# Kernel optimization log

Hardware: AMD Instinct MI355X
Metric: run time of the kernel (lower is better)

The kernel has to match this reference:

```python
import jax, jax.numpy as jnp
import numpy as np

B, N, C, K = 2, 8192, 128, 16
EPS = 1e-5


def setup_inputs() -> dict:
    key = jax.random.key(0)
    ks = jax.random.split(key, 24)
    s = 1.0 / np.sqrt(C)
    nrm = lambda k, shape, sc: jax.random.normal(k, shape, dtype=jnp.float32) * sc
    return {
        "xyz": jax.random.normal(ks[0], (B, N, 3), dtype=jnp.float32),
        "feat": jax.random.normal(ks[1], (B, N, C), dtype=jnp.float32),
        "Wq": nrm(ks[2], (C, C), s),
        "Wk": nrm(ks[3], (C, C), s),
        "Wv": nrm(ks[4], (C, C), s),
        "pW1": nrm(ks[5], (C, 3), 0.5),
        "pb1": nrm(ks[6], (C,), 0.1),
        "pg": jnp.ones((C,), jnp.float32),
        "pbeta": jnp.zeros((C,), jnp.float32),
        "pmean": nrm(ks[7], (C,), 0.1),
        "pvar": jax.random.uniform(ks[8], (C,), jnp.float32, 0.5, 1.5),
        "pW2": nrm(ks[9], (C, C), s),
        "pb2": nrm(ks[10], (C,), 0.1),
        "aW1": nrm(ks[11], (C, C), s),
        "ab1": nrm(ks[12], (C,), 0.1),
        "ag": jnp.ones((C,), jnp.float32),
        "abeta": jnp.zeros((C,), jnp.float32),
        "amean": nrm(ks[13], (C,), 0.1),
        "avar": jax.random.uniform(ks[14], (C,), jnp.float32, 0.5, 1.5),
        "aW2": nrm(ks[15], (C, C), s),
        "ab2": nrm(ks[16], (C,), 0.1),
        "Wout": nrm(ks[17], (C, C), s),
    }


def _bn(x, g, b, mean, var):
    # eval-mode BatchNorm1d with running stats
    return (x - mean) * jax.lax.rsqrt(var + EPS) * g + b


def _lin(x, W):
    # torch nn.Linear convention: W is [out, in]
    return jnp.einsum('...i,oi->...o', x, W)


def reference(xyz, feat, Wq, Wk, Wv, pW1, pb1, pg, pbeta, pmean, pvar, pW2, pb2,
              aW1, ab1, ag, abeta, amean, avar, aW2, ab2, Wout):
    # KNN via squared distances (||a||^2 + ||b||^2 - 2 a.b), [B,N,N]
    sq = jnp.sum(xyz * xyz, axis=-1)
    dist = sq[:, :, None] + sq[:, None, :] - 2.0 * jnp.einsum('bnd,bmd->bnm', xyz, xyz)
    _, idx = jax.lax.top_k(-dist, K)  # [B,N,K] nearest neighbors

    gather = jax.vmap(lambda pts, i: pts[i])  # [B,N,C],[B,N,K] -> [B,N,K,C]
    nb_xyz = gather(xyz, idx)    # [B,N,K,3]
    nb_feat = gather(feat, idx)  # [B,N,K,C]

    q = _lin(feat, Wq)[:, :, None, :]  # [B,N,1,C]
    k = _lin(nb_feat, Wk)              # [B,N,K,C]
    v = _lin(nb_feat, Wv)              # [B,N,K,C]

    rel = nb_xyz - xyz[:, :, None, :]  # [B,N,K,3]
    pos = _lin(jax.nn.relu(_bn(_lin(rel, pW1) + pb1, pg, pbeta, pmean, pvar)), pW2) + pb2

    attn = q - k + pos
    attn = _lin(jax.nn.relu(_bn(_lin(attn, aW1) + ab1, ag, abeta, amean, avar)), aW2) + ab2
    attn = jax.nn.softmax(attn, axis=2)  # per-channel softmax over K neighbors

    out = jnp.sum(attn * (v + pos), axis=2)  # [B,N,C]
    return _lin(out, Wout)
```

## Files before the change

kernel.cpp:

```cpp
#include <hip/hip_runtime.h>
#include <cstdint>
#include <cstddef>

#define BB 2
#define NN 8192
#define CC 128
#define KK 16
#define EPSV 1e-5f
#define GRP 16
#define GPTS 512
#define GCAP 32

typedef unsigned long long u64;
typedef unsigned int u32;
typedef unsigned short ushort_t;
typedef short short8v __attribute__((ext_vector_type(8)));
typedef float f32x4 __attribute__((ext_vector_type(4)));

__device__ __forceinline__ float med3f(float x, float y, float z) {
  float r;
  asm("v_med3_f32 %0, %1, %2, %3" : "=v"(r) : "v"(x), "v"(y), "v"(z));
  return r;
}

__global__ __launch_bounds__(256) void k_prep(const float* __restrict__ xyz,
                                              float4* __restrict__ xyzw) {
  int t = blockIdx.x * 256 + threadIdx.x;
  if (t >= BB * NN) return;
  float x = xyz[t * 3 + 0], y = xyz[t * 3 + 1], z = xyz[t * 3 + 2];
  float sq = __fadd_rn(__fadd_rn(__fmul_rn(x, x), __fmul_rn(y, y)), __fmul_rn(z, z));
  xyzw[t] = make_float4(x, y, z, sq);
}

__device__ __forceinline__ float distf(const float4& q, const float4& c) {
  float dot = __fadd_rn(__fadd_rn(__fmul_rn(q.x, c.x), __fmul_rn(q.y, c.y)),
                        __fmul_rn(q.z, c.z));
  float d = __fsub_rn(__fadd_rn(q.w, c.w), __fmul_rn(2.0f, dot));
  return fmaxf(d, 0.0f);
}

__device__ __forceinline__ float distq(const float4& p, const float4& c) {
  return fmaf(p.z, c.z, fmaf(p.y, c.y, fmaf(p.x, c.x, p.w + c.w)));
}

__global__ __launch_bounds__(256) void k_thr(const float4* __restrict__ xyzw,
                                             float* __restrict__ thr) {
  __shared__ float part[16][16][16];
  const int tid = threadIdx.x;
  const int qloc = tid & 15;
  const int s = tid >> 4;
  const int n = blockIdx.x * 16 + qloc;
  const int b = n >> 13;
  const float4 q = xyzw[n];
  const float4 p = make_float4(-2.f * q.x, -2.f * q.y, -2.f * q.z, q.w);
  const float4* base = xyzw + b * NN;
  float a[KK];
#pragma unroll
  for (int i = 0; i < KK; ++i) a[i] = 3.4e38f;
  const int j0 = s * 64;
#pragma unroll 4
  for (int i = 0; i < 64; ++i) {
    const float4 c = base[(j0 + i) * 8];
    const float d = distq(p, c);
#pragma unroll
    for (int k = KK - 1; k >= 1; --k) a[k] = med3f(d, a[k - 1], a[k]);
    a[0] = fminf(d, a[0]);
  }
#pragma unroll
  for (int i = 0; i < KK; ++i) part[qloc][s][i] = a[i];
  __syncthreads();
  if (s < 4) {
#pragma unroll
    for (int ss = 1; ss < 4; ++ss)
#pragma unroll
      for (int i = 0; i < KK; ++i) {
        const float d = part[qloc][s + ss * 4][i];
#pragma unroll
        for (int k = KK - 1; k >= 1; --k) a[k] = med3f(d, a[k - 1], a[k]);
        a[0] = fminf(d, a[0]);
      }
#pragma unroll
    for (int i = 0; i < KK; ++i) part[qloc][s][i] = a[i];
  }
  __syncthreads();
  if (s == 0) {
#pragma unroll
    for (int ss = 1; ss < 4; ++ss)
#pragma unroll
      for (int i = 0; i < KK; ++i) {
        const float d = part[qloc][ss][i];
#pragma unroll
        for (int k = KK - 1; k >= 1; --k) a[k] = med3f(d, a[k - 1], a[k]);
        a[0] = fminf(d, a[0]);
      }
    const float t = a[KK - 1];
    thr[n] = t + (5e-4f + 4e-5f * fabsf(t));
  }
}

__global__ __launch_bounds__(256) void k_collect(const float4* __restrict__ xyzw,
                                                 const float* __restrict__ thr,
                                                 u32* __restrict__ cnt8,
                                                 u32* __restrict__ list) {
  __shared__ float4 pts[GPTS];
  const int tid = threadIdx.x;
  const int n = blockIdx.x * 256 + tid;
  const int b = n >> 13;
  const int g = blockIdx.y;
  const int m0 = g * GPTS;
#pragma unroll
  for (int i = 0; i < GPTS / 256; ++i)
    pts[i * 256 + tid] = xyzw[b * NN + m0 + i * 256 + tid];
  const float4 q = xyzw[n];
  const float4 p = make_float4(-2.f * q.x, -2.f * q.y, -2.f * q.z, q.w);
  const float tn = thr[n];
  __syncthreads();
  u32* seg = list + ((size_t)n * GRP + g) * GCAP;
  int cnt = 0;
#pragma unroll 4
  for (int mi = 0; mi < GPTS; ++mi) {
    const float d = distq(p, pts[mi]);
    if (d <= tn) {
      if (cnt < GCAP) seg[cnt] = (u32)(m0 + mi);
      ++cnt;
    }
  }
  cnt8[n * GRP + g] = (u32)cnt;
}

__global__ __launch_bounds__(256) void k_fin(const float4* __restrict__ xyzw,
                                             const u32* __restrict__ cnt8,
                                             const u32* __restrict__ list,
                                             int* __restrict__ idx) {
  __shared__ double part[16][16][16];
  const int tid = threadIdx.x;
  const int qloc = tid & 15;
  const int s = tid >> 4;
  const int n = blockIdx.x * 16 + qloc;
  const int b = n >> 13;
  const float4 q = xyzw[n];
  const int cn = (int)cnt8[n * GRP + s];
  const int cl = (cn < GCAP) ? cn : GCAP;
  const u32* L = list + ((size_t)n * GRP + s) * GCAP;
  double keys[KK];
#pragma unroll
  for (int i = 0; i < KK; ++i) keys[i] = __longlong_as_double(0x7FEFFFFFFFFFFFFFLL);
  for (int j = 0; j < cl; ++j) {
    const u32 m = L[j];
    const float d = distf(q, xyzw[b * NN + m]);
    u64 kb_ = ((u64)__float_as_uint(d) << 32) | m;
    double kd = __longlong_as_double((long long)kb_);
    if (kd < keys[KK - 1]) {
#pragma unroll
      for (int i = 0; i < KK; ++i) {
        double lo = fmin(keys[i], kd);
        kd = fmax(keys[i], kd);
        keys[i] = lo;
      }
    }
  }
#pragma unroll
  for (int i = 0; i < KK; ++i) part[qloc][s][i] = keys[i];
  __syncthreads();
  if (s < 4) {
#pragma unroll
    for (int ss = 1; ss < 4; ++ss)
#pragma unroll
      for (int i = 0; i < KK; ++i) {
        double kd = part[qloc][s + ss * 4][i];
        if (kd < keys[KK - 1]) {
#pragma unroll
          for (int k = 0; k < KK; ++k) {
            double lo = fmin(keys[k], kd);
            kd = fmax(keys[k], kd);
            keys[k] = lo;
          }
        }
      }
#pragma unroll
    for (int i = 0; i < KK; ++i) part[qloc][s][i] = keys[i];
  }
  __syncthreads();
  if (s == 0) {
#pragma unroll
    for (int ss = 1; ss < 4; ++ss)
#pragma unroll
      for (int i = 0; i < KK; ++i) {
        double kd = part[qloc][ss][i];
        if (kd < keys[KK - 1]) {
#pragma unroll
          for (int k = 0; k < KK; ++k) {
            double lo = fmin(keys[k], kd);
            kd = fmax(keys[k], kd);
            keys[k] = lo;
          }
        }
      }
    bool ovf = false;
#pragma unroll
    for (int gg = 0; gg < GRP; ++gg) ovf |= (cnt8[n * GRP + gg] > GCAP);
    if (ovf) {
#pragma unroll
      for (int i = 0; i < KK; ++i) keys[i] = __longlong_as_double(0x7FEFFFFFFFFFFFFFLL);
      for (int mi = 0; mi < NN; ++mi) {
        const float d = distf(q, xyzw[b * NN + mi]);
        u64 kb_ = ((u64)__float_as_uint(d) << 32) | (u32)mi;
        double kd = __longlong_as_double((long long)kb_);
        if (kd < keys[KK - 1]) {
#pragma unroll
          for (int k = 0; k < KK; ++k) {
            double lo = fmin(keys[k], kd);
            kd = fmax(keys[k], kd);
            keys[k] = lo;
          }
        }
      }
    }
#pragma unroll
    for (int j = 0; j < KK; ++j)
      idx[n * KK + j] = (int)((u64)__double_as_longlong(keys[j]) & 0xffffffffu);
  }
}

__global__ __launch_bounds__(128) void k_fold(const float* __restrict__ aW1,
                                              const float* __restrict__ Wq,
                                              const float* __restrict__ Wk,
                                              const float* __restrict__ pW2,
                                              const float* __restrict__ pb2,
                                              float* __restrict__ WqA,
                                              float* __restrict__ WkA,
                                              float* __restrict__ WpA,
                                              float* __restrict__ tvec) {
  const int bx = blockIdx.x;
  const int j = threadIdx.x;
  if (bx == 48) {
    float s = 0.f;
    for (int i = 0; i < 128; ++i) s = fmaf(aW1[j * 128 + i], pb2[i], s);
    tvec[j] = s;
    return;
  }
  const int mat = bx >> 4;
  const int c0 = (bx & 15) * 8;
  const float* S = (mat == 0) ? Wq : (mat == 1) ? Wk : pW2;
  float* D = (mat == 0) ? WqA : (mat == 1) ? WkA : WpA;
  float acc[8];
#pragma unroll
  for (int r = 0; r < 8; ++r) acc[r] = 0.f;
  for (int i = 0; i < 128; ++i) {
    float sv = S[i * 128 + j];
#pragma unroll
    for (int r = 0; r < 8; ++r) acc[r] = fmaf(aW1[(c0 + r) * 128 + i], sv, acc[r]);
  }
#pragma unroll
  for (int r = 0; r < 8; ++r) D[(c0 + r) * 128 + j] = acc[r];
}

__device__ __forceinline__ void splitf(float a, ushort_t& h, ushort_t& l) {
  u32 ab = __float_as_uint(a);
  h = (ushort_t)(ab >> 16);
  float hif = __uint_as_float(ab & 0xffff0000u);
  l = (ushort_t)(__float_as_uint(a - hif) >> 16);
}

__global__ __launch_bounds__(256) void k_packw(
    const float* __restrict__ S0, const float* __restrict__ S1,
    const float* __restrict__ S2, const float* __restrict__ S3,
    const float* __restrict__ S4, const float* __restrict__ S5,
    const float* __restrict__ S6, ushort_t* __restrict__ Phall,
    ushort_t* __restrict__ Plall) {
  const int bx = blockIdx.x;
  const int mat = bx >> 3;
  const int T = bx & 7;
  const float* S;
  switch (mat) {
    case 0: S = S0; break;
    case 1: S = S1; break;
    case 2: S = S2; break;
    case 3: S = S3; break;
    case 4: S = S4; break;
    case 5: S = S5; break;
    default: S = S6; break;
  }
  const int tid = threadIdx.x;
  const int s = tid >> 4;
  const int lr = tid & 15;
  const int c = T * 16 + lr;
  short8v vh, vl;
#pragma unroll
  for (int e = 0; e < 8; ++e) {
    ushort_t hh, ll;
    splitf(S[c * 128 + s * 8 + e], hh, ll);
    vh[e] = (short)hh;
    vl[e] = (short)ll;
  }
  const int po = mat * 16384 + T * 2048 + s * 128 + lr * 8;
  *(short8v*)&Phall[po] = vh;
  *(short8v*)&Plall[po] = vl;
}

template <int ITERS>
__device__ __forceinline__ void stage_rows(const float4* __restrict__ G4,
                                           ushort_t* Bh, ushort_t* Bl, int tid) {
#pragma unroll
  for (int i = 0; i < ITERS; ++i) {
    int f = i * 256 + tid;
    int r = f >> 5, k4 = f & 31;
    float4 v = G4[f];
    ushort_t h0, l0, h1, l1, h2, l2, h3, l3;
    splitf(v.x, h0, l0);
    splitf(v.y, h1, l1);
    splitf(v.z, h2, l2);
    splitf(v.w, h3, l3);
    int slot = k4 >> 1;
    int sub = (k4 & 1) * 4;
    int base = r * 128 + ((slot ^ (r & 15)) * 8) + sub;
    *(uint2*)&Bh[base] = make_uint2((u32)h0 | ((u32)h1 << 16), (u32)h2 | ((u32)h3 << 16));
    *(uint2*)&Bl[base] = make_uint2((u32)l0 | ((u32)l1 << 16), (u32)l2 | ((u32)l3 << 16));
  }
}

__device__ __forceinline__ void gemm64g(const ushort_t* ABh, const ushort_t* ABl,
                                        const ushort_t* __restrict__ Ph,
                                        const ushort_t* __restrict__ Pl,
                                        f32x4 acc[2][4], int tid) {
  const int l = tid & 63, wid = tid >> 6;
  const int wrow = wid >> 1, wcol = wid & 1;
  const int lq = l >> 4, lr = l & 15;
#pragma unroll
  for (int ks = 0; ks < 4; ++ks) {
    const int sw8 = (((ks * 4 + lq) ^ lr) * 8);
    short8v ah[2], al[2], wh[4], wl[4];
#pragma unroll
    for (int ct = 0; ct < 4; ++ct) {
      int off = (wcol * 4 + ct) * 2048 + (ks * 4 + lq) * 128 + lr * 8;
      wh[ct] = *(const short8v*)&Ph[off];
      wl[ct] = *(const short8v*)&Pl[off];
    }
#pragma unroll
    for (int rt = 0; rt < 2; ++rt) {
      int row = wrow * 32 + rt * 16 + lr;
      ah[rt] = *(const short8v*)&ABh[row * 128 + sw8];
      al[rt] = *(const short8v*)&ABl[row * 128 + sw8];
    }
    __builtin_amdgcn_s_setprio(1);
#pragma unroll
    for (int rt = 0; rt < 2; ++rt)
#pragma unroll
      for (int ct = 0; ct < 4; ++ct) {
        acc[rt][ct] = __builtin_amdgcn_mfma_f32_16x16x32_bf16(ah[rt], wh[ct], acc[rt][ct], 0, 0, 0);
        acc[rt][ct] = __builtin_amdgcn_mfma_f32_16x16x32_bf16(ah[rt], wl[ct], acc[rt][ct], 0, 0, 0);
        acc[rt][ct] = __builtin_amdgcn_mfma_f32_16x16x32_bf16(al[rt], wh[ct], acc[rt][ct], 0, 0, 0);
      }
    __builtin_amdgcn_s_setprio(0);
  }
}

template <int NW>
__global__ __launch_bounds__(256) void k_mms(const float* __restrict__ A,
                                             const ushort_t* __restrict__ Phall,
                                             const ushort_t* __restrict__ Plall,
                                             int m0, float* __restrict__ C0,
                                             float* __restrict__ C1,
                                             float* __restrict__ C2) {
  __shared__ ushort_t ABh[16 * 128], ABl[16 * 128];
  const int tid = threadIdx.x;
  const int Rbase = blockIdx.x * 16;
  stage_rows<2>((const float4*)(A + (size_t)Rbase * 128), ABh, ABl, tid);
  __syncthreads();
  const int l = tid & 63, wid = tid >> 6;
  const int lq = l >> 4, lr = l & 15;
  float* Cs[3] = {C0, C1, C2};
#pragma unroll
  for (int w = 0; w < NW; ++w) {
    const ushort_t* Ph = Phall + (size_t)(m0 + w) * 16384;
    const ushort_t* Pl = Plall + (size_t)(m0 + w) * 16384;
    f32x4 acc[2];
#pragma unroll
    for (int ct = 0; ct < 2; ++ct) acc[ct] = (f32x4)0.f;
#pragma unroll
    for (int ks = 0; ks < 4; ++ks) {
      const int sw8 = (((ks * 4 + lq) ^ lr) * 8);
      short8v ah, al, wh[2], wl[2];
#pragma unroll
      for (int ct = 0; ct < 2; ++ct) {
        int off = (wid * 2 + ct) * 2048 + (ks * 4 + lq) * 128 + lr * 8;
        wh[ct] = *(const short8v*)&Ph[off];
        wl[ct] = *(const short8v*)&Pl[off];
      }
      ah = *(const short8v*)&ABh[lr * 128 + sw8];
      al = *(const short8v*)&ABl[lr * 128 + sw8];
#pragma unroll
      for (int ct = 0; ct < 2; ++ct) {
        acc[ct] = __builtin_amdgcn_mfma_f32_16x16x32_bf16(ah, wh[ct], acc[ct], 0, 0, 0);
        acc[ct] = __builtin_amdgcn_mfma_f32_16x16x32_bf16(ah, wl[ct], acc[ct], 0, 0, 0);
        acc[ct] = __builtin_amdgcn_mfma_f32_16x16x32_bf16(al, wh[ct], acc[ct], 0, 0, 0);
      }
    }
#pragma unroll
    for (int ct = 0; ct < 2; ++ct) {
      int c = (wid * 2 + ct) * 16 + lr;
#pragma unroll
      for (int reg = 0; reg < 4; ++reg) {
        int R = Rbase + lq * 4 + reg;
        Cs[w][(size_t)R * 128 + c] = acc[ct][reg];
      }
    }
  }
}

__global__ __launch_bounds__(256, 3) void k_fused(
    const float4* __restrict__ xyzw, const int* __restrict__ idx,
    const float* __restrict__ qbA, const float* __restrict__ kbA,
    const float* __restrict__ vb, const float* __restrict__ pW1,
    const float* __restrict__ pb1, const float* __restrict__ pg,
    const float* __restrict__ pbeta, const float* __restrict__ pm,
    const float* __restrict__ pv, const float* __restrict__ pb2,
    const float* __restrict__ ab1, const float* __restrict__ ag,
    const float* __restrict__ abeta, const float* __restrict__ am,
    const float* __restrict__ av, const float* __restrict__ ab2,
    const float* __restrict__ tvec, const ushort_t* __restrict__ Phall,
    const ushort_t* __restrict__ Plall, float* __restrict__ outb) {
  __shared__ ushort_t ABh[64 * 128], ABl[64 * 128];
  __shared__ float4 fW1[128];
  __shared__ float sA[128], tA[128], pB2[128], aB2[128];
  __shared__ int idxs[64];
  const int tid = threadIdx.x;
  const int Qbase = blockIdx.x * 4;
  const int b = Qbase >> 13;

  if (tid < 64) idxs[tid] = idx[Qbase * KK + tid];
  if (tid < 128) {
    int c = tid;
    float s1 = pg[c] / sqrtf(pv[c] + EPSV);
    fW1[c] = make_float4(pW1[c * 3] * s1, pW1[c * 3 + 1] * s1, pW1[c * 3 + 2] * s1,
                         (pb1[c] - pm[c]) * s1 + pbeta[c]);
    float s2 = ag[c] / sqrtf(av[c] + EPSV);
    sA[c] = s2;
    tA[c] = fmaf(s2, ab1[c] + tvec[c] - am[c], abeta[c]);
    pB2[c] = pb2[c];
    aB2[c] = ab2[c];
  }
  __syncthreads();

  {
    int r = tid >> 2, qq = tid & 3;
    int Q = Qbase + (r >> 4);
    int m = idxs[r];
    float4 pq = xyzw[Q];
    float4 pn = xyzw[b * NN + m];
    float rx = pn.x - pq.x, ry = pn.y - pq.y, rz = pn.z - pq.z;
#pragma unroll
    for (int g = 0; g < 4; ++g) {
      short8v vh, vl;
      int c0 = qq * 32 + g * 8;
#pragma unroll
      for (int e = 0; e < 8; ++e) {
        float4 w = fW1[c0 + e];
        float h = fmaxf(fmaf(rz, w.z, fmaf(ry, w.y, fmaf(rx, w.x, w.w))), 0.f);
        ushort_t hh, ll;
        splitf(h, hh, ll);
        vh[e] = (short)hh;
        vl[e] = (short)ll;
      }
      int sw = (c0 >> 3) ^ (r & 15);
      *(short8v*)&ABh[r * 128 + sw * 8] = vh;
      *(short8v*)&ABl[r * 128 + sw * 8] = vl;
    }
  }
  __syncthreads();

  const int l = tid & 63, wid = tid >> 6;
  const int wrow = wid >> 1, wcol = wid & 1;
  const int lq = l >> 4, lr = l & 15;

  f32x4 pos_[2][4], pa_[2][4];
#pragma unroll
  for (int rt = 0; rt < 2; ++rt)
#pragma unroll
    for (int ct = 0; ct < 4; ++ct) {
      pos_[rt][ct] = (f32x4)0.f;
      pa_[rt][ct] = (f32x4)0.f;
    }
  gemm64g(ABh, ABl, Phall, Plall, pos_, tid);
  gemm64g(ABh, ABl, Phall + 16384, Plall + 16384, pa_, tid);
  __syncthreads();

#pragma unroll
  for (int rt = 0; rt < 2; ++rt) {
    int qi_loc = wrow * 2 + rt;
    int Q = Qbase + qi_loc;
    int mr[4];
#pragma unroll
    for (int reg = 0; reg < 4; ++reg) mr[reg] = b * NN + idxs[qi_loc * 16 + lq * 4 + reg];
#pragma unroll
    for (int ct = 0; ct < 4; ++ct) {
      int c = wcol * 64 + ct * 16 + lr;
      float qv = qbA[(size_t)Q * 128 + c];
      float sc = sA[c], tc = tA[c];
#pragma unroll
      for (int reg = 0; reg < 4; ++reg) {
        float u = qv - kbA[(size_t)mr[reg] * 128 + c] + pa_[rt][ct][reg];
        float z = fmaxf(fmaf(u, sc, tc), 0.f);
        ushort_t hh, ll;
        splitf(z, hh, ll);
        int R15 = lq * 4 + reg;
        int row = wrow * 32 + rt * 16 + R15;
        int base = row * 128 + (((c >> 3) ^ R15) * 8) + (c & 7);
        ABh[base] = hh;
        ABl[base] = ll;
      }
    }
  }
  __syncthreads();

  f32x4 acc[2][4];
#pragma unroll
  for (int rt = 0; rt < 2; ++rt)
#pragma unroll
    for (int ct = 0; ct < 4; ++ct) acc[rt][ct] = (f32x4)0.f;
  gemm64g(ABh, ABl, Phall + 32768, Plall + 32768, acc, tid);

#pragma unroll
  for (int rt = 0; rt < 2; ++rt) {
    int qi_loc = wrow * 2 + rt;
    int Q = Qbase + qi_loc;
    int mr[4];
#pragma unroll
    for (int reg = 0; reg < 4; ++reg) mr[reg] = b * NN + idxs[qi_loc * 16 + lq * 4 + reg];
#pragma unroll
    for (int ct = 0; ct < 4; ++ct) {
      int c = wcol * 64 + ct * 16 + lr;
      float ab2v = aB2[c];
      float lg[4];
#pragma unroll
      for (int reg = 0; reg < 4; ++reg) lg[reg] = acc[rt][ct][reg] + ab2v;
      float mx = fmaxf(fmaxf(lg[0], lg[1]), fmaxf(lg[2], lg[3]));
      mx = fmaxf(mx, __shfl_xor(mx, 16));
      mx = fmaxf(mx, __shfl_xor(mx, 32));
      float s = 0.f, o = 0.f;
      float pb2v = pB2[c];
#pragma unroll
      for (int reg = 0; reg < 4; ++reg) {
        float e_ = expf(lg[reg] - mx);
        s += e_;
        float vv = vb[(size_t)mr[reg] * 128 + c] + pos_[rt][ct][reg] + pb2v;
        o = fmaf(e_, vv, o);
      }
      s += __shfl_xor(s, 16);
      s += __shfl_xor(s, 32);
      o += __shfl_xor(o, 16);
      o += __shfl_xor(o, 32);
      if (lq == 0) outb[(size_t)Q * 128 + c] = o / s;
    }
  }
}

extern "C" void kernel_launch(void* const* d_in, const int* in_sizes, int n_in,
                              void* d_out, int out_size, void* d_ws, size_t ws_size,
                              hipStream_t stream) {
  const float* xyz = (const float*)d_in[0];
  const float* feat = (const float*)d_in[1];
  const float* Wq = (const float*)d_in[2];
  const float* Wk = (const float*)d_in[3];
  const float* Wv = (const float*)d_in[4];
  const float* pW1 = (const float*)d_in[5];
  const float* pb1 = (const float*)d_in[6];
  const float* pg = (const float*)d_in[7];
  const float* pbeta = (const float*)d_in[8];
  const float* pmean = (const float*)d_in[9];
  const float* pvar = (const float*)d_in[10];
  const float* pW2 = (const float*)d_in[11];
  const float* pb2 = (const float*)d_in[12];
  const float* aW1 = (const float*)d_in[13];
  const float* ab1 = (const float*)d_in[14];
  const float* ag = (const float*)d_in[15];
  const float* abeta = (const float*)d_in[16];
  const float* amean = (const float*)d_in[17];
  const float* avar = (const float*)d_in[18];
  const float* aW2 = (const float*)d_in[19];
  const float* ab2 = (const float*)d_in[20];
  const float* Wout = (const float*)d_in[21];
  float* out = (float*)d_out;
  char* ws = (char*)d_ws;

  size_t off = 0;
  auto alloc = [&](size_t bytes) {
    size_t r = off;
    off += (bytes + 255) & ~(size_t)255;
    return r;
  };
  float4* xyzw = (float4*)(ws + alloc((size_t)BB * NN * 16));
  int* idx = (int*)(ws + alloc((size_t)BB * NN * KK * 4));
  size_t o_qb = alloc((size_t)BB * NN * CC * 4);
  size_t o_kb = alloc((size_t)BB * NN * CC * 4);
  size_t o_vb = alloc((size_t)BB * NN * CC * 4);
  size_t o_ob = alloc((size_t)BB * NN * CC * 4);
  float* qbA = (float*)(ws + o_qb);
  float* kbA = (float*)(ws + o_kb);
  float* vb = (float*)(ws + o_vb);
  float* outb = (float*)(ws + o_ob);
  u32* list = (u32*)(ws + o_qb);
  float* WqA = (float*)(ws + alloc(128 * 128 * 4));
  float* WkA = (float*)(ws + alloc(128 * 128 * 4));
  float* WpA = (float*)(ws + alloc(128 * 128 * 4));
  float* tvec = (float*)(ws + alloc(128 * 4));
  ushort_t* Phall = (ushort_t*)(ws + alloc(7 * 16384 * 2));
  ushort_t* Plall = (ushort_t*)(ws + alloc(7 * 16384 * 2));
  float* thrbuf = (float*)(ws + alloc((size_t)BB * NN * 4));
  u32* cnt8 = (u32*)(ws + alloc((size_t)BB * NN * GRP * 4));

  k_prep<<<(BB * NN) / 256, 256, 0, stream>>>(xyz, xyzw);
  k_fold<<<49, 128, 0, stream>>>(aW1, Wq, Wk, pW2, pb2, WqA, WkA, WpA, tvec);
  k_packw<<<56, 256, 0, stream>>>(pW2, WpA, aW2, WqA, WkA, Wv, Wout, Phall, Plall);

  k_thr<<<(BB * NN) / 16, 256, 0, stream>>>(xyzw, thrbuf);
  k_collect<<<dim3((BB * NN) / 256, GRP), 256, 0, stream>>>(xyzw, thrbuf, cnt8, list);
  k_fin<<<(BB * NN) / 16, 256, 0, stream>>>(xyzw, cnt8, list, idx);

  k_mms<3><<<(BB * NN) / 16, 256, 0, stream>>>(feat, Phall, Plall, 3, qbA, kbA, vb);

  k_fused<<<(BB * NN * KK) / 64, 256, 0, stream>>>(
      xyzw, idx, qbA, kbA, vb, pW1, pb1, pg, pbeta, pmean, pvar, pb2, ab1, ag,
      abeta, amean, avar, ab2, tvec, Phall, Plall, outb);

  k_mms<1><<<(BB * NN) / 16, 256, 0, stream>>>(outb, Phall, Plall, 6, out, nullptr,
                                               nullptr);
}
```

Measured before the change: 247.8 us.

## Fuse final Wout projection into the attention kernel epilogue

The per-query attention outputs now go into shared memory as split bf16 hi/lo values instead of a global scratch buffer. Each block then runs a small MFMA GEMM against the packed Wout weights and writes the final output directly. This drops the separate k_mms<1> launch and the write-then-read of the intermediate outb buffer. In exchange, the 16x16 MFMA tile carries only 4 valid query rows, so most of its work is wasted, and two extra block-wide barriers are added.

```diff
diff --git a/kernel.cpp b/kernel.cpp
--- a/kernel.cpp
+++ b/kernel.cpp
@@ -419,7 +419,7 @@
     const float* __restrict__ abeta, const float* __restrict__ am,
     const float* __restrict__ av, const float* __restrict__ ab2,
     const float* __restrict__ tvec, const ushort_t* __restrict__ Phall,
-    const ushort_t* __restrict__ Plall, float* __restrict__ outb) {
+    const ushort_t* __restrict__ Plall, float* __restrict__ out) {
   __shared__ ushort_t ABh[64 * 128], ABl[64 * 128];
   __shared__ float4 fW1[128];
   __shared__ float sA[128], tA[128], pB2[128], aB2[128];
@@ -520,10 +520,10 @@
     for (int ct = 0; ct < 4; ++ct) acc[rt][ct] = (f32x4)0.f;
   gemm64g(ABh, ABl, Phall + 32768, Plall + 32768, acc, tid);
 
+  float oo[2][4];
 #pragma unroll
   for (int rt = 0; rt < 2; ++rt) {
     int qi_loc = wrow * 2 + rt;
-    int Q = Qbase + qi_loc;
     int mr[4];
 #pragma unroll
     for (int reg = 0; reg < 4; ++reg) mr[reg] = b * NN + idxs[qi_loc * 16 + lq * 4 + reg];
@@ -550,7 +550,55 @@
       s += __shfl_xor(s, 32);
       o += __shfl_xor(o, 16);
       o += __shfl_xor(o, 32);
-      if (lq == 0) outb[(size_t)Q * 128 + c] = o / s;
+      oo[rt][ct] = o / s;
+    }
+  }
+
+  __syncthreads();
+  if (lq == 0) {
+#pragma unroll
+    for (int rt = 0; rt < 2; ++rt) {
+      int row = wrow * 2 + rt;
+#pragma unroll
+      for (int ct = 0; ct < 4; ++ct) {
+        int c = wcol * 64 + ct * 16 + lr;
+        ushort_t hh, ll;
+        splitf(oo[rt][ct], hh, ll);
+        int base = row * 128 + (((c >> 3) ^ row) * 8) + (c & 7);
+        ABh[base] = hh;
+        ABl[base] = ll;
+      }
+    }
+  }
+  __syncthreads();
+
+  const ushort_t* Ph6 = Phall + 6 * 16384;
+  const ushort_t* Pl6 = Plall + 6 * 16384;
+  f32x4 fo[2];
+  fo[0] = (f32x4)0.f;
+  fo[1] = (f32x4)0.f;
+#pragma unroll
+  for (int ks = 0; ks < 4; ++ks) {
+    const int sw8 = (((ks * 4 + lq) ^ lr) * 8);
+    short8v ah = *(const short8v*)&ABh[lr * 128 + sw8];
+    short8v al = *(const short8v*)&ABl[lr * 128 + sw8];
+#pragma unroll
+    for (int ct = 0; ct < 2; ++ct) {
+      int off2 = (wid * 2 + ct) * 2048 + (ks * 4 + lq) * 128 + lr * 8;
+      short8v wh = *(const short8v*)&Ph6[off2];
+      short8v wl = *(const short8v*)&Pl6[off2];
+      fo[ct] = __builtin_amdgcn_mfma_f32_16x16x32_bf16(ah, wh, fo[ct], 0, 0, 0);
+      fo[ct] = __builtin_amdgcn_mfma_f32_16x16x32_bf16(ah, wl, fo[ct], 0, 0, 0);
+      fo[ct] = __builtin_amdgcn_mfma_f32_16x16x32_bf16(al, wh, fo[ct], 0, 0, 0);
+    }
+  }
+  if (lq == 0) {
+#pragma unroll
+    for (int ct = 0; ct < 2; ++ct) {
+      int c = (wid * 2 + ct) * 16 + lr;
+#pragma unroll
+      for (int reg = 0; reg < 4; ++reg)
+        out[(size_t)(Qbase + reg) * 128 + c] = fo[ct][reg];
     }
   }
 }
@@ -598,7 +646,7 @@
   float* qbA = (float*)(ws + o_qb);
   float* kbA = (float*)(ws + o_kb);
   float* vb = (float*)(ws + o_vb);
-  float* outb = (float*)(ws + o_ob);
+  (void)o_ob;
   u32* list = (u32*)(ws + o_qb);
   float* WqA = (float*)(ws + alloc(128 * 128 * 4));
   float* WkA = (float*)(ws + alloc(128 * 128 * 4));
@@ -621,8 +669,5 @@
 
   k_fused<<<(BB * NN * KK) / 64, 256, 0, stream>>>(
       xyzw, idx, qbA, kbA, vb, pW1, pb1, pg, pbeta, pmean, pvar, pb2, ab1, ag,
-      abeta, amean, avar, ab2, tvec, Phall, Plall, outb);
-
-  k_mms<1><<<(BB * NN) / 16, 256, 0, stream>>>(outb, Phall, Plall, 6, out, nullptr,
-                                               nullptr);
-}
+      abeta, amean, avar, ab2, tvec, Phall, Plall, out);
+}
```

After: 248.8 us. Within noise of the previous version (+0.4%).
